# Kernel optimization log

Hardware: AMD Instinct MI355X
Metric: run time of the kernel (lower is better)

The kernel has to match this reference:

```python
import jax, jax.numpy as jnp
import numpy as np

B, N, C = 8, 4096, 320
HEAD, SR = 5, 2
HEAD_DIM = C // HEAD
SCALE = HEAD_DIM ** -0.5
LN_EPS = 1e-5


def setup_inputs() -> dict:
    key = jax.random.key(0)
    ks = jax.random.split(key, 8)
    s = 0.02
    return {
        "x": jax.random.normal(ks[0], (B, N, C), jnp.float32),
        "q_w": jax.random.normal(ks[1], (C, C), jnp.float32) * s,
        "q_b": jnp.zeros((C,), jnp.float32),
        "kv_w": jax.random.normal(ks[2], (C, 2 * C), jnp.float32) * s,
        "kv_b": jnp.zeros((2 * C,), jnp.float32),
        "sr_w": jax.random.normal(ks[3], (SR, SR, C, C), jnp.float32) * s,  # HWIO
        "sr_b": jnp.zeros((C,), jnp.float32),
        "ln_g": jnp.ones((C,), jnp.float32),
        "ln_b": jnp.zeros((C,), jnp.float32),
        "proj_w": jax.random.normal(ks[4], (C, C), jnp.float32) * s,
        "proj_b": jnp.zeros((C,), jnp.float32),
        "H": 64,
        "W": 64,
    }


def reference(x, q_w, q_b, kv_w, kv_b, sr_w, sr_b, ln_g, ln_b, proj_w, proj_b, H, W):
    b, n, c = x.shape
    # q projection -> [B, head, N, d]
    q = (x @ q_w + q_b).reshape(b, n, HEAD, HEAD_DIM).transpose(0, 2, 1, 3)
    # spatial reduction of KV: strided conv (kernel=stride=SR) + LayerNorm
    x_img = x.reshape(b, H, W, c)  # NHWC
    x_ = jax.lax.conv_general_dilated(
        x_img, sr_w, window_strides=(SR, SR), padding="VALID",
        dimension_numbers=("NHWC", "HWIO", "NHWC")) + sr_b
    x_ = x_.reshape(b, -1, c)  # [B, N/SR^2, C]
    mu = jnp.mean(x_, axis=-1, keepdims=True)
    var = jnp.mean(jnp.square(x_ - mu), axis=-1, keepdims=True)
    x_ = (x_ - mu) * jax.lax.rsqrt(var + LN_EPS) * ln_g + ln_b
    # kv projection -> k, v each [B, head, Nkv, d]
    kv = (x_ @ kv_w + kv_b).reshape(b, -1, 2, HEAD, HEAD_DIM)
    k = kv[:, :, 0].transpose(0, 2, 1, 3)
    v = kv[:, :, 1].transpose(0, 2, 1, 3)
    # attention
    attn = jnp.einsum("bhnd,bhmd->bhnm", q, k) * SCALE
    attn = jax.nn.softmax(attn, axis=-1)
    out = jnp.einsum("bhnm,bhmd->bhnd", attn, v)
    out = out.transpose(0, 2, 1, 3).reshape(b, n, c)
    return out @ proj_w + proj_b
```

## Files before the change

kernel.cpp:

```cpp
#include <hip/hip_runtime.h>

typedef __attribute__((ext_vector_type(8))) short bf16x8;
typedef __attribute__((ext_vector_type(4))) short bf16x4;
typedef __attribute__((ext_vector_type(4))) float f32x4;
typedef __attribute__((ext_vector_type(2))) float f32x2;
typedef __attribute__((ext_vector_type(2))) unsigned u32x2;
typedef __attribute__((ext_vector_type(4))) unsigned u32x4;

#define DEVI static __device__ __forceinline__
#define AS1 __attribute__((address_space(1)))
#define AS3 __attribute__((address_space(3)))

DEVI unsigned short f2bf(float f) {
  unsigned u = __builtin_bit_cast(unsigned, f);
  return (unsigned short)((u + 0x7FFFu + ((u >> 16) & 1u)) >> 16);
}

DEVI unsigned pkbf(float a, float b) {
#if __has_builtin(__builtin_amdgcn_cvt_pk_bf16_f32)
  return __builtin_bit_cast(unsigned, __builtin_amdgcn_cvt_pk_bf16_f32(a, b));
#else
  return (unsigned)f2bf(a) | ((unsigned)f2bf(b) << 16);
#endif
}

DEVI float fast_exp2(float x) {
#if __has_builtin(__builtin_amdgcn_exp2f)
  return __builtin_amdgcn_exp2f(x);
#else
  return exp2f(x);
#endif
}

DEVI void gl_lds16(const unsigned short* g, unsigned short* l) {
  __builtin_amdgcn_global_load_lds((const AS1 unsigned int*)g, (AS3 unsigned int*)l, 16, 0, 0);
}

DEVI size_t frag_off(int row, int k, int KG) {
  return ((size_t)(row >> 4) * KG + (k >> 3)) * 128 + (row & 15) * 8 + (k & 7);
}

__global__ __launch_bounds__(256)
void k_prep(const float* __restrict__ x, unsigned short* __restrict__ xf) {
  __shared__ __align__(16) unsigned short L[20480];
  const int t = threadIdx.x;
  const size_t base = (size_t)blockIdx.x * 64 * 320;
#pragma unroll
  for (int i = 0; i < 10; i++) {
    int c = i * 256 + t;
    const float* p = x + base + (size_t)c * 8;
    f32x4 a = ((const f32x4*)p)[0], b = ((const f32x4*)p)[1];
    u32x4 pk = {pkbf(a[0], a[1]), pkbf(a[2], a[3]), pkbf(b[0], b[1]), pkbf(b[2], b[3])};
    int r = c / 40, g = c - r * 40;
    int gidx = ((r >> 4) * 40 + g) * 16 + (r & 15);
    int sidx = gidx ^ ((gidx >> 4) & 7);
    *(u32x4*)(L + sidx * 8) = pk;
  }
  __syncthreads();
  unsigned short* outb = xf + base;
#pragma unroll
  for (int i = 0; i < 10; i++) {
    int o = i * 256 + t;
    int sidx = o ^ ((o >> 4) & 7);
    *(u32x4*)(outb + (size_t)o * 8) = *(const u32x4*)(L + sidx * 8);
  }
}

__global__ __launch_bounds__(256)
void k_transpose_all(const float* __restrict__ q_w, const float* __restrict__ kv_w,
                     const float* __restrict__ proj_w, const float* __restrict__ sr_w,
                     unsigned short* __restrict__ Wq, unsigned short* __restrict__ Wkv,
                     unsigned short* __restrict__ Wp, unsigned short* __restrict__ Wsr) {
  const float* src; unsigned short* dst; int K, N;
  switch (blockIdx.z) {
    case 0:  src = q_w;    dst = Wq;  K = 320;  N = 320; break;
    case 1:  src = kv_w;   dst = Wkv; K = 320;  N = 640; break;
    case 2:  src = proj_w; dst = Wp;  K = 320;  N = 320; break;
    default: src = sr_w;   dst = Wsr; K = 1280; N = 320; break;
  }
  if ((int)blockIdx.x >= (K >> 5) || (int)blockIdx.y >= (N >> 5)) return;
  const int KG = K >> 3;
  __shared__ float tile[32][33];
  const int k0 = blockIdx.x * 32, n0 = blockIdx.y * 32;
  const int tx = threadIdx.x, ty = threadIdx.y;
#pragma unroll
  for (int i = 0; i < 4; i++)
    tile[ty + i * 8][tx] = src[(size_t)(k0 + ty + i * 8) * N + n0 + tx];
  __syncthreads();
#pragma unroll
  for (int i = 0; i < 4; i++) {
    int n = n0 + ty + i * 8, k = k0 + tx;
    dst[frag_off(n, k, KG)] = f2bf(tile[tx][ty + i * 8]);
  }
}

__global__ __launch_bounds__(256)
void k_ln(const float* __restrict__ xc, const float* __restrict__ gam,
          const float* __restrict__ bet, unsigned short* __restrict__ xr) {
  const int row = blockIdx.x * 4 + (threadIdx.x >> 6);
  const int l = threadIdx.x & 63;
  const float* p = xc + (size_t)row * 320;
  float s = 0.f, ss = 0.f;
#pragma unroll
  for (int i = 0; i < 5; i++) { float v = p[l + 64 * i]; s += v; ss += v * v; }
#pragma unroll
  for (int o = 1; o < 64; o <<= 1) { s += __shfl_xor(s, o); ss += __shfl_xor(ss, o); }
  float mu = s * (1.f / 320.f);
  float var = ss * (1.f / 320.f) - mu * mu;
  float rstd = rsqrtf(var + 1e-5f);
  if (l < 40) {
    f32x4 a = ((const f32x4*)(p + l * 8))[0], b = ((const f32x4*)(p + l * 8))[1];
    f32x4 ga = ((const f32x4*)(gam + l * 8))[0], gb = ((const f32x4*)(gam + l * 8))[1];
    f32x4 ba = ((const f32x4*)(bet + l * 8))[0], bb = ((const f32x4*)(bet + l * 8))[1];
    f32x4 ya, yb;
#pragma unroll
    for (int j = 0; j < 4; j++) {
      ya[j] = (a[j] - mu) * rstd * ga[j] + ba[j];
      yb[j] = (b[j] - mu) * rstd * gb[j] + bb[j];
    }
    u32x4 pk = {pkbf(ya[0], ya[1]), pkbf(ya[2], ya[3]), pkbf(yb[0], yb[1]), pkbf(yb[2], yb[3])};
    *(u32x4*)(xr + ((size_t)((row >> 4) * 40 + l)) * 128 + (row & 15) * 8) = pk;
  }
}

template <int MT, int AK, int EPI, int NSEG>
__global__ __launch_bounds__(256)
void k_gemm(const unsigned short* __restrict__ A, const unsigned short* __restrict__ W,
            const float* __restrict__ bias, void* __restrict__ outp, void* __restrict__ outp2,
            float oscale) {
  __shared__ __align__(16) unsigned short Bl[20480];
  const int t = threadIdx.x, w = t >> 6, ln = t & 63, lr = ln & 15, lq = ln >> 4;
  const int m0 = blockIdx.x * (MT * 64), n0 = blockIdx.y * 64;

  f32x4 acc[MT][4];
#pragma unroll
  for (int i = 0; i < MT; i++)
#pragma unroll
    for (int j = 0; j < 4; j++) acc[i][j] = (f32x4){0.f, 0.f, 0.f, 0.f};

  int crt[MT], crow[MT];
  if (AK == 1) {
#pragma unroll
    for (int mi = 0; mi < MT; mi++) {
      int gm = m0 + (w * MT + mi) * 16;
      int b = gm >> 10, p = gm & 1023, oy = p >> 5, ox0 = p & 31;
      crt[mi] = b * 256 + ((2 * oy) * 64 + 2 * ox0) >> 4;
      crow[mi] = 0;
      (void)crow[mi];
    }
  }

#pragma unroll
  for (int seg = 0; seg < NSEG; seg++) {
    const int kh = seg >> 1, kw = seg & 1;
    if (seg) __syncthreads();
    if (AK == 0) {
      const unsigned short* Ws = W + ((size_t)(n0 >> 4) * 40) * 128;
#pragma unroll
      for (int j = 0; j < 10; j++)
        gl_lds16(Ws + (size_t)(j * 4 + w) * 512 + ln * 8, Bl + (j * 4 + w) * 512);
    } else {
      const unsigned short* Wt = W + ((size_t)((n0 >> 4) + w) * 160 + seg * 40) * 128;
#pragma unroll
      for (int j = 0; j < 10; j++)
        gl_lds16(Wt + (size_t)j * 512 + ln * 8, Bl + w * 5120 + j * 512);
    }
    __syncthreads();

#pragma unroll
    for (int ks = 0; ks < 10; ks++) {
      bf16x8 af[MT], bfr[4];
#pragma unroll
      for (int mi = 0; mi < MT; mi++) {
        if (AK == 0) {
          af[mi] = *(const bf16x8*)(
              A + ((size_t)((m0 >> 4) + w * MT + mi) * 40 + ks * 4 + lq) * 128 + lr * 8);
        } else {
          int gm = m0 + (w * MT + mi) * 16;
          int b = gm >> 10, p = gm & 1023, oy = p >> 5, ox0 = p & 31;
          int r0 = (2 * oy + kh) * 64 + 2 * ox0 + kw;
          int brt = b * 256 + (r0 >> 4);
          af[mi] = *(const bf16x8*)(
              A + ((size_t)(brt + (lr >> 3)) * 40 + ks * 4 + lq) * 128 +
              (kw + 2 * (lr & 7)) * 8);
        }
      }
#pragma unroll
      for (int ni = 0; ni < 4; ni++)
        bfr[ni] = *(const bf16x8*)(Bl + ((ni * 40) + ks * 4 + lq) * 128 + lr * 8);
#pragma unroll
      for (int mi = 0; mi < MT; mi++)
#pragma unroll
        for (int ni = 0; ni < 4; ni++)
          acc[mi][ni] =
              __builtin_amdgcn_mfma_f32_16x16x32_bf16(af[mi], bfr[ni], acc[mi][ni], 0, 0, 0);
    }
  }

  if (EPI == 0) {
    unsigned short* out = (unsigned short*)outp;
    const int h = n0 >> 6;
#pragma unroll
    for (int mi = 0; mi < MT; mi++)
#pragma unroll
      for (int ni = 0; ni < 4; ni++)
#pragma unroll
        for (int rr = 0; rr < 4; rr++) {
          int gm = m0 + (w * MT + mi) * 16 + lq * 4 + rr;
          int b = gm >> 12, n = gm & 4095, d = ni * 16 + lr;
          out[((size_t)(b * 5 + h) << 18) + ((size_t)n << 6) + d] =
              f2bf((acc[mi][ni][rr] + bias[n0 + d]) * oscale);
        }
  } else if (EPI == 3) {
    float* out = (float*)outp;
#pragma unroll
    for (int mi = 0; mi < MT; mi++)
#pragma unroll
      for (int ni = 0; ni < 4; ni++)
#pragma unroll
        for (int rr = 0; rr < 4; rr++) {
          int gm = m0 + (w * MT + mi) * 16 + lq * 4 + rr;
          int gc = n0 + ni * 16 + lr;
          out[(size_t)gm * 320 + gc] = acc[mi][ni][rr] + bias[gc];
        }
  } else {
    if (n0 < 320) {
      unsigned short* out = (unsigned short*)outp;
      const int h = n0 >> 6;
#pragma unroll
      for (int mi = 0; mi < MT; mi++)
#pragma unroll
        for (int ni = 0; ni < 4; ni++)
#pragma unroll
          for (int rr = 0; rr < 4; rr++) {
            int gm = m0 + (w * MT + mi) * 16 + lq * 4 + rr;
            int b = gm >> 10, mm = gm & 1023, d = ni * 16 + lr;
            out[((size_t)(b * 5 + h) << 16) + ((size_t)mm << 6) + d] =
                f2bf(acc[mi][ni][rr] + bias[n0 + d]);
          }
    } else {
      unsigned short* out = (unsigned short*)outp2;
      const int h = (n0 - 320) >> 6;
      unsigned short* Tl = (unsigned short*)Bl;
      __syncthreads();
#pragma unroll
      for (int mi = 0; mi < MT; mi++)
#pragma unroll
        for (int ni = 0; ni < 4; ni++)
#pragma unroll
          for (int rr = 0; rr < 4; rr++) {
            int ml = (w * MT + mi) * 16 + lq * 4 + rr;
            int d = ni * 16 + lr;
            Tl[d * 136 + ml] = f2bf(acc[mi][ni][rr] + bias[n0 + d]);
          }
      __syncthreads();
      const int b = m0 >> 10, mm0 = m0 & 1023;
#pragma unroll
      for (int i = 0; i < 4; i++) {
        int ch = t + 256 * i, d = ch >> 4, g = ch & 15;
        *(bf16x8*)(out + ((size_t)(b * 5 + h) << 16) + d * 1024 + mm0 + g * 8) =
            *(const bf16x8*)(Tl + d * 136 + g * 8);
      }
    }
  }
}

__global__ __launch_bounds__(256)
void k_attn(const unsigned short* __restrict__ Qb, const unsigned short* __restrict__ Kb,
            const unsigned short* __restrict__ Vt, unsigned short* __restrict__ AO) {
  __shared__ __align__(16) unsigned char smem[32768];
  const int t = threadIdx.x, w = t >> 6, ln = t & 63, lr = ln & 15, lq = ln >> 4;
  const int bh = blockIdx.y;
  const int m0 = blockIdx.x * 128 + w * 32;
  const unsigned short* Qp = Qb + ((size_t)bh << 18);
  const unsigned short* Kp = Kb + ((size_t)bh << 16);
  const unsigned short* Vp = Vt + ((size_t)bh << 16);

  bf16x8 qf[2][2];
#pragma unroll
  for (int mt = 0; mt < 2; mt++)
#pragma unroll
    for (int t2 = 0; t2 < 2; t2++)
      qf[mt][t2] = *(const bf16x8*)(Qp + (size_t)(m0 + mt * 16 + lr) * 64 + t2 * 32 + lq * 8);

  f32x4 oacc[4][2];
  f32x2 den2[2] = {(f32x2){0.f, 0.f}, (f32x2){0.f, 0.f}};
#pragma unroll
  for (int dt = 0; dt < 4; dt++)
#pragma unroll
    for (int mt = 0; mt < 2; mt++) oacc[dt][mt] = (f32x4){0.f, 0.f, 0.f, 0.f};

  const int rS = ln >> 3, sS = ln & 7;

  auto stage = [&](int c, int buf) {
    unsigned short* KL = (unsigned short*)(smem + buf * 16384);
    unsigned short* VL = KL + 4096;
#pragma unroll
    for (int i = 0; i < 2; i++) {
      int r = (w * 2 + i) * 8 + rS;
      int g = sS ^ (r & 7);
      gl_lds16(Kp + (size_t)(c * 64 + r) * 64 + g * 8, KL + (w * 2 + i) * 512);
      gl_lds16(Vp + (size_t)r * 1024 + c * 64 + g * 8, VL + (w * 2 + i) * 512);
    }
  };

  stage(0, 0);
  __syncthreads();

  for (int c = 0; c < 16; c++) {
    if (c < 15) stage(c + 1, (c + 1) & 1);
    const unsigned short* KL = (const unsigned short*)(smem + (c & 1) * 16384);
    const unsigned short* VL = KL + 4096;

    f32x4 sacc[4][2];
#pragma unroll
    for (int kt = 0; kt < 4; kt++) {
      int kr = 16 * kt + lr;
      bf16x8 kf0 = *(const bf16x8*)(KL + kr * 64 + ((lq ^ (lr & 7)) * 8));
      bf16x8 kf1 = *(const bf16x8*)(KL + kr * 64 + (((4 + lq) ^ (lr & 7)) * 8));
#pragma unroll
      for (int mt = 0; mt < 2; mt++) {
        f32x4 s = (f32x4){0.f, 0.f, 0.f, 0.f};
        s = __builtin_amdgcn_mfma_f32_16x16x32_bf16(kf0, qf[mt][0], s, 0, 0, 0);
        s = __builtin_amdgcn_mfma_f32_16x16x32_bf16(kf1, qf[mt][1], s, 0, 0, 0);
        sacc[kt][mt] = s;
      }
    }

#pragma unroll
    for (int tp = 0; tp < 2; tp++) {
      bf16x8 pf8[2];
#pragma unroll
      for (int mt = 0; mt < 2; mt++) {
        f32x4 ea, eb;
#pragma unroll
        for (int j = 0; j < 4; j++) {
          ea[j] = fast_exp2(sacc[2 * tp][mt][j]);
          eb[j] = fast_exp2(sacc[2 * tp + 1][mt][j]);
        }
        den2[mt] += (f32x2){ea[0], ea[1]} + (f32x2){ea[2], ea[3]};
        den2[mt] += (f32x2){eb[0], eb[1]} + (f32x2){eb[2], eb[3]};
        u32x4 pk = {pkbf(ea[0], ea[1]), pkbf(ea[2], ea[3]),
                    pkbf(eb[0], eb[1]), pkbf(eb[2], eb[3])};
        pf8[mt] = __builtin_bit_cast(bf16x8, pk);
      }
#pragma unroll
      for (int dt = 0; dt < 4; dt++) {
        int vr = dt * 16 + lr;
        const unsigned short* vbase = VL + vr * 64;
        int ga = 4 * tp + (lq >> 1), gb = ga + 2;
        bf16x4 vlo = *(const bf16x4*)(vbase + (ga ^ (lr & 7)) * 8 + (lq & 1) * 4);
        bf16x4 vhi = *(const bf16x4*)(vbase + (gb ^ (lr & 7)) * 8 + (lq & 1) * 4);
        bf16x8 vf8 = {vlo[0], vlo[1], vlo[2], vlo[3], vhi[0], vhi[1], vhi[2], vhi[3]};
#pragma unroll
        for (int mt = 0; mt < 2; mt++)
          oacc[dt][mt] =
              __builtin_amdgcn_mfma_f32_16x16x32_bf16(vf8, pf8[mt], oacc[dt][mt], 0, 0, 0);
      }
    }
    __syncthreads();
  }

  float inv[2];
#pragma unroll
  for (int mt = 0; mt < 2; mt++) {
    float s = den2[mt][0] + den2[mt][1];
    s += __shfl_xor(s, 16);
    s += __shfl_xor(s, 32);
    inv[mt] = 1.f / s;
  }

  const int b = bh / 5, h = bh - b * 5;
  const int rt0 = b * 256 + (m0 >> 4);
#pragma unroll
  for (int mt = 0; mt < 2; mt++)
#pragma unroll
    for (int dt = 0; dt < 4; dt++) {
      float i0 = inv[mt];
      u32x2 pk = {pkbf(oacc[dt][mt][0] * i0, oacc[dt][mt][1] * i0),
                  pkbf(oacc[dt][mt][2] * i0, oacc[dt][mt][3] * i0)};
      int colg = h * 8 + dt * 2 + (lq >> 1);
      size_t off = ((size_t)(rt0 + mt) * 40 + colg) * 128 + lr * 8 + (lq & 1) * 4;
      *(u32x2*)(AO + off) = pk;
    }
}

extern "C" void kernel_launch(void* const* d_in, const int* in_sizes, int n_in,
                              void* d_out, int out_size, void* d_ws, size_t ws_size,
                              hipStream_t stream) {
  (void)in_sizes; (void)n_in; (void)out_size; (void)ws_size;
  const float* x      = (const float*)d_in[0];
  const float* q_w    = (const float*)d_in[1];
  const float* q_b    = (const float*)d_in[2];
  const float* kv_w   = (const float*)d_in[3];
  const float* kv_b   = (const float*)d_in[4];
  const float* sr_w   = (const float*)d_in[5];
  const float* sr_b   = (const float*)d_in[6];
  const float* ln_g   = (const float*)d_in[7];
  const float* ln_b   = (const float*)d_in[8];
  const float* proj_w = (const float*)d_in[9];
  const float* proj_b = (const float*)d_in[10];
  float* out = (float*)d_out;

  char* ws = (char*)d_ws;
  size_t off = 0;
  auto alloc = [&](size_t bytes) {
    void* p = ws + off;
    off += (bytes + 255) & ~(size_t)255;
    return p;
  };
  unsigned short* xbf_fr = (unsigned short*)alloc((size_t)32768 * 320 * 2);
  unsigned short* Qb     = (unsigned short*)alloc((size_t)32768 * 320 * 2);
  unsigned short* KbP    = (unsigned short*)alloc((size_t)40 * 65536 * 2);
  unsigned short* VtP    = (unsigned short*)alloc((size_t)40 * 65536 * 2);
  float*          xc     = (float*)alloc((size_t)8192 * 320 * 4);
  unsigned short* xr     = (unsigned short*)alloc((size_t)8192 * 320 * 2);
  unsigned short* Wq_fr  = (unsigned short*)alloc((size_t)320 * 320 * 2);
  unsigned short* Wkv_fr = (unsigned short*)alloc((size_t)640 * 320 * 2);
  unsigned short* Wp_fr  = (unsigned short*)alloc((size_t)320 * 320 * 2);
  unsigned short* Wsr_fr = (unsigned short*)alloc((size_t)320 * 1280 * 2);
  unsigned short* AO = xbf_fr;

  const float S2 = 0.125f * 1.4426950408889634f;

  k_prep<<<512, 256, 0, stream>>>(x, xbf_fr);
  k_transpose_all<<<dim3(40, 20, 4), dim3(32, 8), 0, stream>>>(
      q_w, kv_w, proj_w, sr_w, Wq_fr, Wkv_fr, Wp_fr, Wsr_fr);

  k_gemm<2, 1, 3, 4><<<dim3(64, 5), 256, 0, stream>>>(xbf_fr, Wsr_fr, sr_b, xc, nullptr, 1.f);
  k_ln<<<2048, 256, 0, stream>>>(xc, ln_g, ln_b, xr);
  k_gemm<4, 0, 0, 1><<<dim3(128, 5), 256, 0, stream>>>(xbf_fr, Wq_fr, q_b, Qb, nullptr, S2);
  k_gemm<2, 0, 4, 1><<<dim3(64, 10), 256, 0, stream>>>(xr, Wkv_fr, kv_b, KbP, VtP, 1.f);
  k_attn<<<dim3(32, 40), 256, 0, stream>>>(Qb, KbP, VtP, AO);
  k_gemm<4, 0, 3, 1><<<dim3(128, 5), 256, 0, stream>>>(AO, Wp_fr, proj_b, out, nullptr, 1.f);
}
```

Before: 228.2 us.

## Compute softmax denominator via MFMA with ones and vectorize V fragment loads

The attention kernel now accumulates the softmax denominator with an extra MFMA against a ones vector, replacing per-lane VALU adds and the cross-lane shuffle reduction, and uses a hardware reciprocal. V fragments are read with a single 16-byte LDS load instead of two 8-byte loads, which changes which keys each lane pairs with and must match the P fragment layout. The KV GEMM epilogue's transpose store reorders its LDS reads to match, and dead conv index code is removed. The risk is a mismatch between the reordered K/V permutation and the bf16-rounded denominator, which lowers precision somewhat.

```diff
diff --git a/kernel.cpp b/kernel.cpp
--- a/kernel.cpp
+++ b/kernel.cpp
@@ -29,6 +29,14 @@
   return __builtin_amdgcn_exp2f(x);
 #else
   return exp2f(x);
+#endif
+}
+
+DEVI float fast_rcp(float x) {
+#if __has_builtin(__builtin_amdgcn_rcpf)
+  return __builtin_amdgcn_rcpf(x);
+#else
+  return 1.f / x;
 #endif
 }
 
@@ -137,18 +145,6 @@
   for (int i = 0; i < MT; i++)
 #pragma unroll
     for (int j = 0; j < 4; j++) acc[i][j] = (f32x4){0.f, 0.f, 0.f, 0.f};
-
-  int crt[MT], crow[MT];
-  if (AK == 1) {
-#pragma unroll
-    for (int mi = 0; mi < MT; mi++) {
-      int gm = m0 + (w * MT + mi) * 16;
-      int b = gm >> 10, p = gm & 1023, oy = p >> 5, ox0 = p & 31;
-      crt[mi] = b * 256 + ((2 * oy) * 64 + 2 * ox0) >> 4;
-      crow[mi] = 0;
-      (void)crow[mi];
-    }
-  }
 
 #pragma unroll
   for (int seg = 0; seg < NSEG; seg++) {
@@ -258,8 +254,12 @@
 #pragma unroll
       for (int i = 0; i < 4; i++) {
         int ch = t + 256 * i, d = ch >> 4, g = ch & 15;
-        *(bf16x8*)(out + ((size_t)(b * 5 + h) << 16) + d * 1024 + mm0 + g * 8) =
-            *(const bf16x8*)(Tl + d * 136 + g * 8);
+        int c2 = g >> 2, ns = g & 3;
+        const unsigned short* src = Tl + d * 136 + c2 * 32 + ns * 4;
+        bf16x4 lo = *(const bf16x4*)(src);
+        bf16x4 hi = *(const bf16x4*)(src + 16);
+        bf16x8 v8 = {lo[0], lo[1], lo[2], lo[3], hi[0], hi[1], hi[2], hi[3]};
+        *(bf16x8*)(out + ((size_t)(b * 5 + h) << 16) + d * 1024 + mm0 + g * 8) = v8;
       }
     }
   }
@@ -283,8 +283,12 @@
     for (int t2 = 0; t2 < 2; t2++)
       qf[mt][t2] = *(const bf16x8*)(Qp + (size_t)(m0 + mt * 16 + lr) * 64 + t2 * 32 + lq * 8);
 
+  bf16x8 ones8;
+#pragma unroll
+  for (int j = 0; j < 8; j++) ones8[j] = (short)0x3F80;
+
   f32x4 oacc[4][2];
-  f32x2 den2[2] = {(f32x2){0.f, 0.f}, (f32x2){0.f, 0.f}};
+  f32x4 dacc[2] = {(f32x4){0.f, 0.f, 0.f, 0.f}, (f32x4){0.f, 0.f, 0.f, 0.f}};
 #pragma unroll
   for (int dt = 0; dt < 4; dt++)
 #pragma unroll
@@ -338,20 +342,15 @@
           ea[j] = fast_exp2(sacc[2 * tp][mt][j]);
           eb[j] = fast_exp2(sacc[2 * tp + 1][mt][j]);
         }
-        den2[mt] += (f32x2){ea[0], ea[1]} + (f32x2){ea[2], ea[3]};
-        den2[mt] += (f32x2){eb[0], eb[1]} + (f32x2){eb[2], eb[3]};
         u32x4 pk = {pkbf(ea[0], ea[1]), pkbf(ea[2], ea[3]),
                     pkbf(eb[0], eb[1]), pkbf(eb[2], eb[3])};
         pf8[mt] = __builtin_bit_cast(bf16x8, pk);
+        dacc[mt] = __builtin_amdgcn_mfma_f32_16x16x32_bf16(ones8, pf8[mt], dacc[mt], 0, 0, 0);
       }
 #pragma unroll
       for (int dt = 0; dt < 4; dt++) {
         int vr = dt * 16 + lr;
-        const unsigned short* vbase = VL + vr * 64;
-        int ga = 4 * tp + (lq >> 1), gb = ga + 2;
-        bf16x4 vlo = *(const bf16x4*)(vbase + (ga ^ (lr & 7)) * 8 + (lq & 1) * 4);
-        bf16x4 vhi = *(const bf16x4*)(vbase + (gb ^ (lr & 7)) * 8 + (lq & 1) * 4);
-        bf16x8 vf8 = {vlo[0], vlo[1], vlo[2], vlo[3], vhi[0], vhi[1], vhi[2], vhi[3]};
+        bf16x8 vf8 = *(const bf16x8*)(VL + vr * 64 + (((4 * tp + lq) ^ (lr & 7)) * 8));
 #pragma unroll
         for (int mt = 0; mt < 2; mt++)
           oacc[dt][mt] =
@@ -363,12 +362,7 @@
 
   float inv[2];
 #pragma unroll
-  for (int mt = 0; mt < 2; mt++) {
-    float s = den2[mt][0] + den2[mt][1];
-    s += __shfl_xor(s, 16);
-    s += __shfl_xor(s, 32);
-    inv[mt] = 1.f / s;
-  }
+  for (int mt = 0; mt < 2; mt++) inv[mt] = fast_rcp(dacc[mt][0]);
 
   const int b = bh / 5, h = bh - b * 5;
   const int rt0 = b * 256 + (m0 >> 4);
```

Result: slower. 238.2 us (+4.4%).
